# Optimization experiments

Hardware: AMD Instinct MI355X
Metric: run time of the kernel (lower is better)

Reference implementation:

```python
import jax, jax.numpy as jnp
import numpy as np

B, ID, OD = 4096, 2048, 1024


def _conv_softmax(x, w):
    # x: [..., L]; torch Conv1d(1,1,k=3,stride=1,pad=1,bias=False) then softmax(dim=-1)
    L = x.shape[-1]
    xp = jnp.pad(x, [(0, 0)] * (x.ndim - 1) + [(1, 1)])
    y = w[0] * xp[..., 0:L] + w[1] * xp[..., 1:L + 1] + w[2] * xp[..., 2:L + 2]
    return jax.nn.softmax(y, axis=-1)


def _lstm_cell(x, h, c, Wih, Whh, bih, bhh):
    # torch LSTMCell gate order: i, f, g, o
    g = x @ Wih.T + h @ Whh.T + (bih + bhh)
    i, f, gg, o = jnp.split(g, 4, axis=-1)
    c2 = jax.nn.sigmoid(f) * c + jax.nn.sigmoid(i) * jnp.tanh(gg)
    h2 = jax.nn.sigmoid(o) * jnp.tanh(c2)
    return h2, c2


def _lstm_params(key, in_dim, hid):
    k = 1.0 / np.sqrt(hid)
    ks = jax.random.split(key, 4)
    Wih = jax.random.uniform(ks[0], (4 * hid, in_dim), jnp.float32, -k, k)
    Whh = jax.random.uniform(ks[1], (4 * hid, hid), jnp.float32, -k, k)
    bih = jax.random.uniform(ks[2], (4 * hid,), jnp.float32, -k, k)
    bhh = jax.random.uniform(ks[3], (4 * hid,), jnp.float32, -k, k)
    return Wih, Whh, bih, bhh


def setup_inputs() -> dict:
    key = jax.random.key(0)
    ks = jax.random.split(key, 12)
    spec = jax.random.normal(ks[0], (B, ID), jnp.float32)
    Wih1, Whh1, bih1, bhh1 = _lstm_params(ks[1], ID, OD)
    Wih2, Whh2, bih2, bhh2 = _lstm_params(ks[2], ID // 2, OD // 2)
    Wih3, Whh3, bih3, bhh3 = _lstm_params(ks[3], ID // 4, OD // 4)
    Wih4, Whh4, bih4, bhh4 = _lstm_params(ks[4], ID // 8, OD // 8)
    ck = np.sqrt(1.0 / 3.0)  # Conv1d(1,1,3) init bound
    w2_1h = jax.random.uniform(ks[5], (3,), jnp.float32, -ck, ck)
    w2_1c = jax.random.uniform(ks[6], (3,), jnp.float32, -ck, ck)
    w3_2h = jax.random.uniform(ks[7], (3,), jnp.float32, -ck, ck)
    w3_2c = jax.random.uniform(ks[8], (3,), jnp.float32, -ck, ck)
    w4_3h = jax.random.uniform(ks[9], (3,), jnp.float32, -ck, ck)
    w4_3c = jax.random.uniform(ks[10], (3,), jnp.float32, -ck, ck)
    return dict(spec=spec,
                Wih1=Wih1, Whh1=Whh1, bih1=bih1, bhh1=bhh1,
                Wih2=Wih2, Whh2=Whh2, bih2=bih2, bhh2=bhh2,
                Wih3=Wih3, Whh3=Whh3, bih3=bih3, bhh3=bhh3,
                Wih4=Wih4, Whh4=Whh4, bih4=bih4, bhh4=bhh4,
                w2_1h=w2_1h, w2_1c=w2_1c, w3_2h=w3_2h, w3_2c=w3_2c,
                w4_3h=w4_3h, w4_3c=w4_3c)


def reference(spec, Wih1, Whh1, bih1, bhh1, Wih2, Whh2, bih2, bhh2,
              Wih3, Whh3, bih3, bhh3, Wih4, Whh4, bih4, bhh4,
              w2_1h, w2_1c, w3_2h, w3_2c, w4_3h, w4_3c):
    b = spec.shape[0]
    # Level 4: 8 independent steps, fresh zero state each (torch code passes no hidden)
    x4 = spec.reshape(b, 8, ID // 8)
    z4 = jnp.zeros((b, 8, OD // 8), spec.dtype)
    h4, c4 = _lstm_cell(x4, z4, z4, Wih4, Whh4, bih4, bhh4)   # [b,8,OD/8]
    hb4 = _conv_softmax(h4.reshape(b, 4, OD // 4), w4_3h)      # pairs -> [b,4,OD/4]
    cb4 = _conv_softmax(c4.reshape(b, 4, OD // 4), w4_3c)
    # Level 3: 4 independent steps seeded by level-4 blended states
    x3 = spec.reshape(b, 4, ID // 4)
    h3, c3 = _lstm_cell(x3, hb4, cb4, Wih3, Whh3, bih3, bhh3)  # [b,4,OD/4]
    hb3 = _conv_softmax(h3.reshape(b, 2, OD // 2), w3_2h)      # [b,2,OD/2]
    cb3 = _conv_softmax(c3.reshape(b, 2, OD // 2), w3_2c)
    # Level 2: 2 independent steps
    x2 = spec.reshape(b, 2, ID // 2)
    h2, c2 = _lstm_cell(x2, hb3, cb3, Wih2, Whh2, bih2, bhh2)  # [b,2,OD/2]
    hb2 = _conv_softmax(h2.reshape(b, OD), w2_1h)              # [b,OD]
    cb2 = _conv_softmax(c2.reshape(b, OD), w2_1c)
    # Level 1: single full-resolution step; forward returns out1 = h1
    h1, c1 = _lstm_cell(spec, hb2, cb2, Wih1, Whh1, bih1, bhh1)
    return h1
```

## Files before the change

### kernel.cpp

```cpp
#include <hip/hip_runtime.h>


typedef __bf16 bf16x8 __attribute__((ext_vector_type(8)));
typedef float f32x4 __attribute__((ext_vector_type(4)));
typedef unsigned short u16x4 __attribute__((ext_vector_type(4)));
typedef unsigned short u16x8 __attribute__((ext_vector_type(8)));

#define AS1 __attribute__((address_space(1)))
#define AS3 __attribute__((address_space(3)))

__device__ __forceinline__ unsigned short f2bf(float f) {
    union { float f; unsigned int i; } v; v.f = f;
    unsigned int r = v.i + 0x7fffu + ((v.i >> 16) & 1u);
    return (unsigned short)(r >> 16);
}
__device__ __forceinline__ float bf2f(unsigned short u) {
    union { unsigned int i; float f; } v; v.i = ((unsigned int)u) << 16; return v.f;
}
__device__ __forceinline__ float sigm(float x) { return 1.f / (1.f + __expf(-x)); }
__device__ __forceinline__ float tanh_(float x) { float e = __expf(2.f * x); return 1.f - 2.f / (e + 1.f); }

__global__ __launch_bounds__(256) void cvt_spec4(
    const float* __restrict__ spec, unsigned short* __restrict__ sB,
    unsigned short* __restrict__ X, unsigned short* __restrict__ Y,
    unsigned short* __restrict__ Z, long n4)
{
    const long stride = (long)gridDim.x * blockDim.x;
    for (long i = (long)blockIdx.x * blockDim.x + threadIdx.x; i < n4; i += stride) {
        const float4 v = ((const float4*)spec)[i];
        u16x4 o; o.x = f2bf(v.x); o.y = f2bf(v.y); o.z = f2bf(v.z); o.w = f2bf(v.w);
        ((u16x4*)sB)[i] = o;
        const long b = i >> 9;
        const int c4 = (int)(i & 511);
        *(u16x4*)(X + (b * 4 + (c4 >> 7)) * 768  + ((c4 & 127) << 2)) = o;
        *(u16x4*)(Y + (b * 2 + (c4 >> 8)) * 1536 + ((c4 & 255) << 2)) = o;
        *(u16x4*)(Z + b * 3072 + (c4 << 2)) = o;
    }
}

struct PSeg { const float* src; unsigned short* dst; long g0; int H; int kshift; int dstld; int dstcol; };
struct PArgs { PSeg s[7]; long total; };

__global__ __launch_bounds__(256) void cvt_permW_all(PArgs pa)
{
    const long stride = (long)gridDim.x * blockDim.x;
    for (long gi = (long)blockIdx.x * blockDim.x + threadIdx.x; gi < pa.total; gi += stride) {
        int si = 0;
#pragma unroll
        for (int k = 1; k < 7; ++k) si += (gi >= pa.s[k].g0);
        const PSeg sg = pa.s[si];
        const long i = gi - sg.g0;
        const int kq = 1 << sg.kshift;
        const int p = (int)(i >> sg.kshift);
        const int kk = ((int)i & (kq - 1)) << 2;
        const int o = ((p >> 6) << 4) | (p & 15);
        const int q = (p >> 4) & 3;
        const long r = (long)q * sg.H + o;
        const float4 v = *(const float4*)(sg.src + (r << (sg.kshift + 2)) + kk);
        u16x4 wv; wv.x = f2bf(v.x); wv.y = f2bf(v.y); wv.z = f2bf(v.z); wv.w = f2bf(v.w);
        *(u16x4*)(sg.dst + (long)p * sg.dstld + sg.dstcol + kk) = wv;
    }
}

__global__ __launch_bounds__(256) void bias_all(
    const float* __restrict__ bih1, const float* __restrict__ bhh1,
    const float* __restrict__ bih2, const float* __restrict__ bhh2,
    const float* __restrict__ bih3, const float* __restrict__ bhh3,
    const float* __restrict__ bih4, const float* __restrict__ bhh4,
    float* __restrict__ bs1, float* __restrict__ bs2,
    float* __restrict__ bs3, float* __restrict__ bs4)
{
    const int i = blockIdx.x * 256 + threadIdx.x;
    const float *bih, *bhh; float* dst; int H, j;
    if (i < 4096)      { bih = bih1; bhh = bhh1; dst = bs1; H = 1024; j = i; }
    else if (i < 6144) { bih = bih2; bhh = bhh2; dst = bs2; H = 512;  j = i - 4096; }
    else if (i < 7168) { bih = bih3; bhh = bhh3; dst = bs3; H = 256;  j = i - 6144; }
    else               { bih = bih4; bhh = bhh4; dst = bs4; H = 128;  j = i - 7168; }
    const int o = ((j >> 6) << 4) | (j & 15);
    const int q = (j >> 4) & 3;
    dst[j] = bih[q * H + o] + bhh[q * H + o];
}

#define QUAD(AF, S, NS, BF)                                                                 \
    { _Pragma("unroll") for (int mi = 0; mi < 4; ++mi) {                                    \
        _Pragma("unroll") for (int ni = 0; ni < 2; ++ni) {                                  \
            acc[(S)*4+mi][(NS)*2+ni] = __builtin_amdgcn_mfma_f32_16x16x32_bf16(             \
                AF[mi][0], BF[ni][0], acc[(S)*4+mi][(NS)*2+ni], 0, 0, 0);                   \
            acc[(S)*4+mi][(NS)*2+ni] = __builtin_amdgcn_mfma_f32_16x16x32_bf16(             \
                AF[mi][1], BF[ni][1], acc[(S)*4+mi][(NS)*2+ni], 0, 0, 0);                   \
    } } }

#define GLL(gsrc, loff) __builtin_amdgcn_global_load_lds(                                   \
    (const AS1 void*)(gsrc), (AS3 void*)(lds + (loff)), 16, 0, 0)

#define FENCE asm volatile("" ::: "memory")

template<bool HAS_CIN, bool LAST>
__global__ __launch_bounds__(512, 2) void gemm8(
    const unsigned short* __restrict__ A, const unsigned short* __restrict__ W, const int K,
    const float* __restrict__ bsum, const unsigned short* __restrict__ Cin,
    float* __restrict__ HoutF, unsigned short* __restrict__ HoutB,
    unsigned short* __restrict__ CoutB, const int H)
{
    __shared__ __align__(16) char lds[131072];
    const int t = threadIdx.x;
    const int w = t >> 6, l = t & 63;
    const int wr = w >> 2, wc = w & 3;

    const int GX = gridDim.x, GY = gridDim.y;
    const int nwg = GX * GY;
    const int bid = (int)blockIdx.y * GX + (int)blockIdx.x;
    const int swz = (bid & 7) * (nwg >> 3) + (bid >> 3);
    const int m0 = (swz / GY) * 256, n0 = (swz % GY) * 256;

    const int colsw = ((l & 7) ^ (l >> 3)) * 8;
    const size_t k128 = (size_t)128 * K;
    const size_t aoff0 = (size_t)(m0 + w * 16 + (l >> 3)) * K + colsw;
    const size_t aoff1 = aoff0 + (size_t)8 * K;
    const size_t boff0 = (size_t)(n0 + w * 16 + (l >> 3)) * K + colsw;
    const size_t boff1 = boff0 + (size_t)8 * K;
    const int sd0 = w * 2048 + l * 16;
    const int sd1 = sd0 + 1024;

    const int lr128 = (l & 15) * 128;
    const int sw0 = (((l >> 4)    ) ^ (l & 7)) * 16;
    const int sw1 = (((l >> 4) + 4) ^ (l & 7)) * 16;

    f32x4 acc[8][4];
#pragma unroll
    for (int i = 0; i < 8; ++i)
#pragma unroll
        for (int j = 0; j < 4; ++j) acc[i][j] = (f32x4){0.f, 0.f, 0.f, 0.f};

    const int NT = K >> 6;

    GLL(A + aoff0, sd0);                      GLL(A + aoff1, sd1);
    GLL(A + aoff0 + k128, 16384 + sd0);       GLL(A + aoff1 + k128, 16384 + sd1);
    GLL(W + boff0, 32768 + sd0);              GLL(W + boff1, 32768 + sd1);
    GLL(W + boff0 + k128, 49152 + sd0);       GLL(W + boff1 + k128, 49152 + sd1);
    GLL(W + boff0 + 64, 98304 + sd0);         GLL(W + boff1 + 64, 98304 + sd1);
    GLL(W + boff0 + k128 + 64, 114688 + sd0); GLL(W + boff1 + k128 + 64, 114688 + sd1);

    bf16x8 aLo[4][2], aHi[4][2], bF0[2][2], bF1[2][2];

    for (int tt = 0; tt < NT; ++tt) {
        const int q = tt & 1, qn = q ^ 1;
        const int rbA = (q << 16) + (wr << 14) + lr128;
        const int rbB = (q << 16) + 32768 + wc * 8192 + lr128;
        const bool st1 = (tt + 1 < NT), st2 = (tt + 2 < NT);

        if (st1) { asm volatile("s_waitcnt vmcnt(4)" ::: "memory"); }
        else     { asm volatile("s_waitcnt vmcnt(0)" ::: "memory"); }
        __builtin_amdgcn_s_barrier();
        FENCE;

#pragma unroll
        for (int mi = 0; mi < 4; ++mi) {
            aLo[mi][0] = *(const bf16x8*)(lds + rbA + mi * 2048 + sw0);
            aLo[mi][1] = *(const bf16x8*)(lds + rbA + mi * 2048 + sw1);
        }
#pragma unroll
        for (int ni = 0; ni < 2; ++ni) {
            bF0[ni][0] = *(const bf16x8*)(lds + rbB + ni * 2048 + sw0);
            bF0[ni][1] = *(const bf16x8*)(lds + rbB + ni * 2048 + sw1);
            bF1[ni][0] = *(const bf16x8*)(lds + rbB + 4096 + ni * 2048 + sw0);
            bF1[ni][1] = *(const bf16x8*)(lds + rbB + 4096 + ni * 2048 + sw1);
        }
        if (st1) {
            const size_t ko1 = (size_t)(tt + 1) * 64;
            GLL(A + aoff0 + ko1, (qn << 16) + sd0);
            GLL(A + aoff1 + ko1, (qn << 16) + sd1);
            GLL(A + aoff0 + k128 + ko1, (qn << 16) + 16384 + sd0);
            GLL(A + aoff1 + k128 + ko1, (qn << 16) + 16384 + sd1);
        }
#pragma unroll
        for (int mi = 0; mi < 4; ++mi) {
            aHi[mi][0] = *(const bf16x8*)(lds + rbA + 8192 + mi * 2048 + sw0);
            aHi[mi][1] = *(const bf16x8*)(lds + rbA + 8192 + mi * 2048 + sw1);
        }

        __builtin_amdgcn_s_setprio(1);
        QUAD(aLo, 0, 0, bF0);
        QUAD(aLo, 0, 1, bF1);
        __builtin_amdgcn_s_setprio(0);
        __builtin_amdgcn_s_barrier();
        FENCE;

        if (st2) {
            const size_t ko2 = (size_t)(tt + 2) * 64;
            GLL(W + boff0 + ko2, (q << 16) + 32768 + sd0);
            GLL(W + boff1 + ko2, (q << 16) + 32768 + sd1);
            GLL(W + boff0 + k128 + ko2, (q << 16) + 49152 + sd0);
            GLL(W + boff1 + k128 + ko2, (q << 16) + 49152 + sd1);
        }
        __builtin_amdgcn_s_setprio(1);
        QUAD(aHi, 1, 1, bF1);
        QUAD(aHi, 1, 0, bF0);
        __builtin_amdgcn_s_setprio(0);
    }

    const int ocol = (n0 >> 6) * 16 + wc * 16 + (l & 15);
    const int bb = n0 + wc * 64 + (l & 15);
    const float b0 = bsum[bb], b1 = bsum[bb + 16], b2 = bsum[bb + 32], b3 = bsum[bb + 48];
    const int mrow0 = m0 + wr * 128 + (l >> 4) * 4;
#pragma unroll
    for (int mi = 0; mi < 8; ++mi)
#pragma unroll
        for (int j = 0; j < 4; ++j) {
            const size_t m = (size_t)(mrow0 + mi * 16 + j);
            const float gi = acc[mi][0][j] + b0;
            const float gf = acc[mi][1][j] + b1;
            const float gg = acc[mi][2][j] + b2;
            const float go = acc[mi][3][j] + b3;
            float c2 = sigm(gi) * tanh_(gg);
            if (HAS_CIN) c2 += sigm(gf) * bf2f(Cin[m * H + ocol]);
            const float h2 = sigm(go) * tanh_(c2);
            if (LAST) {
                HoutF[m * H + ocol] = h2;
            } else {
                HoutB[m * H + ocol] = f2bf(h2);
                CoutB[m * H + ocol] = f2bf(c2);
            }
        }
}

template<int L>
__global__ __launch_bounds__(256) void conv_dual(
    const unsigned short* __restrict__ Hin, const unsigned short* __restrict__ Cin,
    const float* __restrict__ w3h, const float* __restrict__ w3c,
    unsigned short* __restrict__ Yb, int ldYb, unsigned short* __restrict__ cbuf)
{
    constexpr int R = 2048 / L;
    constexpr int TPR = L / 8;
    __shared__ float xs[R][L + 2];
    __shared__ float red[8];
    const int nb = gridDim.x >> 1;
    const bool isC = (int)blockIdx.x >= nb;
    const int row0 = (isC ? (int)blockIdx.x - nb : (int)blockIdx.x) * R;
    const unsigned short* Xs = isC ? Cin : Hin;
    const float* w3 = isC ? w3c : w3h;
    const int t = threadIdx.x;
    const int r = t / TPR;
    const int c8 = (t % TPR) * 8;
    const float w0 = w3[0], w1 = w3[1], w2 = w3[2];

    const u16x8 v = *(const u16x8*)(Xs + (size_t)(row0 + r) * L + c8);
#pragma unroll
    for (int k = 0; k < 8; ++k) xs[r][c8 + 1 + k] = bf2f(v[k]);
    if (t < R) { xs[t][0] = 0.f; xs[t][L + 1] = 0.f; }
    __syncthreads();

    float y[8];
    float vmax = -3.4e38f;
#pragma unroll
    for (int k = 0; k < 8; ++k) {
        y[k] = w0 * xs[r][c8 + k] + w1 * xs[r][c8 + k + 1] + w2 * xs[r][c8 + k + 2];
        vmax = fmaxf(vmax, y[k]);
    }
#pragma unroll
    for (int off = (TPR >= 64 ? 32 : TPR / 2); off >= 1; off >>= 1)
        vmax = fmaxf(vmax, __shfl_xor(vmax, off));
    if (TPR == 128) {
        if ((t & 63) == 0) red[t >> 6] = vmax;
        __syncthreads();
        vmax = fmaxf(red[2 * r], red[2 * r + 1]);
    }
    float s = 0.f;
#pragma unroll
    for (int k = 0; k < 8; ++k) { y[k] = __expf(y[k] - vmax); s += y[k]; }
#pragma unroll
    for (int off = (TPR >= 64 ? 32 : TPR / 2); off >= 1; off >>= 1)
        s += __shfl_xor(s, off);
    if (TPR == 128) {
        if ((t & 63) == 0) red[4 + (t >> 6)] = s;
        __syncthreads();
        s = red[4 + 2 * r] + red[4 + 2 * r + 1];
    }
    const float inv = 1.f / s;
    u16x8 o;
#pragma unroll
    for (int k = 0; k < 8; ++k) o[k] = f2bf(y[k] * inv);
    if (isC) *(u16x8*)(cbuf + (size_t)(row0 + r) * L + c8) = o;
    else     *(u16x8*)(Yb + (size_t)(row0 + r) * ldYb + c8) = o;
}

extern "C" void kernel_launch(void* const* d_in, const int* in_sizes, int n_in,
                              void* d_out, int out_size, void* d_ws, size_t ws_size,
                              hipStream_t stream)
{
    (void)in_sizes; (void)n_in; (void)out_size; (void)ws_size;
    const float* spec  = (const float*)d_in[0];
    const float* Wih1  = (const float*)d_in[1];
    const float* Whh1  = (const float*)d_in[2];
    const float* bih1  = (const float*)d_in[3];
    const float* bhh1  = (const float*)d_in[4];
    const float* Wih2  = (const float*)d_in[5];
    const float* Whh2  = (const float*)d_in[6];
    const float* bih2  = (const float*)d_in[7];
    const float* bhh2  = (const float*)d_in[8];
    const float* Wih3  = (const float*)d_in[9];
    const float* Whh3  = (const float*)d_in[10];
    const float* bih3  = (const float*)d_in[11];
    const float* bhh3  = (const float*)d_in[12];
    const float* Wih4  = (const float*)d_in[13];
    const float* bih4  = (const float*)d_in[15];
    const float* bhh4  = (const float*)d_in[16];
    const float* w2_1h = (const float*)d_in[17];
    const float* w2_1c = (const float*)d_in[18];
    const float* w3_2h = (const float*)d_in[19];
    const float* w3_2c = (const float*)d_in[20];
    const float* w4_3h = (const float*)d_in[21];
    const float* w4_3c = (const float*)d_in[22];

    char* ws = (char*)d_ws;
    unsigned short* h   = (unsigned short*)(ws + 0);
    unsigned short* c   = (unsigned short*)(ws + (size_t)8388608);
    unsigned short* cb  = (unsigned short*)(ws + (size_t)16777216);
    unsigned short* sB  = (unsigned short*)(ws + (size_t)25165824);
    unsigned short* X   = (unsigned short*)(ws + (size_t)41943040);
    unsigned short* Y   = (unsigned short*)(ws + (size_t)67108864);
    unsigned short* Z   = (unsigned short*)(ws + (size_t)92274688);
    unsigned short* Wc1 = (unsigned short*)(ws + (size_t)117440512);
    unsigned short* Wc2 = (unsigned short*)(ws + (size_t)142606336);
    unsigned short* Wc3 = (unsigned short*)(ws + (size_t)148897792);
    unsigned short* W4  = (unsigned short*)(ws + (size_t)150470656);
    float*          bs1 = (float*)(ws + (size_t)150732800);
    float*          bs2 = bs1 + 4096;
    float*          bs3 = bs2 + 4096;
    float*          bs4 = bs3 + 4096;

    cvt_spec4<<<2048, 256, 0, stream>>>(spec, sB, X, Y, Z, 2097152);
    PArgs pa;
    pa.s[0] = { Wih1, Wc1,       0, 1024, 9, 3072,    0 };
    pa.s[1] = { Whh1, Wc1, 2097152, 1024, 8, 3072, 2048 };
    pa.s[2] = { Wih2, Wc2, 3145728,  512, 8, 1536,    0 };
    pa.s[3] = { Whh2, Wc2, 3670016,  512, 7, 1536, 1024 };
    pa.s[4] = { Wih3, Wc3, 3932160,  256, 7,  768,    0 };
    pa.s[5] = { Whh3, Wc3, 4063232,  256, 6,  768,  512 };
    pa.s[6] = { Wih4, W4,  4128768,  128, 6,  256,    0 };
    pa.total = 4161536;
    cvt_permW_all<<<2048, 256, 0, stream>>>(pa);
    bias_all<<<30, 256, 0, stream>>>(bih1, bhh1, bih2, bhh2, bih3, bhh3, bih4, bhh4,
                                     bs1, bs2, bs3, bs4);

    gemm8<false, false><<<dim3(128, 2), 512, 0, stream>>>(sB, W4, 256, bs4, nullptr,
                                                          nullptr, h, c, 128);
    conv_dual<256><<<4096, 256, 0, stream>>>(h, c, w4_3h, w4_3c, X + 512, 768, cb);

    gemm8<true, false><<<dim3(64, 4), 512, 0, stream>>>(X, Wc3, 768, bs3, cb,
                                                        nullptr, h, c, 256);
    conv_dual<512><<<4096, 256, 0, stream>>>(h, c, w3_2h, w3_2c, Y + 1024, 1536, cb);

    gemm8<true, false><<<dim3(32, 8), 512, 0, stream>>>(Y, Wc2, 1536, bs2, cb,
                                                        nullptr, h, c, 512);
    conv_dual<1024><<<4096, 256, 0, stream>>>(h, c, w2_1h, w2_1c, Z + 2048, 3072, cb);

    gemm8<true, true><<<dim3(16, 16), 512, 0, stream>>>(Z, Wc1, 3072, bs1, cb,
                                                        (float*)d_out, nullptr, nullptr, 1024);
}
```

Baseline: 277.8 us.

## Read GEMM A operand from two sources instead of materialised concatenated buffers

The GEMM now takes two A pointers, spec in bf16 and the blended hidden state, and picks the source per K tile. This removes the X/Y/Z concatenation copies of spec and the strided writes into them. The spec conversion, weight permutation and bias summation are also merged into a single prep kernel, cutting two launches. The trade is extra branching and address arithmetic in the GEMM staging loop.

```diff
diff --git a/kernel.cpp b/kernel.cpp
--- a/kernel.cpp
+++ b/kernel.cpp
@@ -20,74 +20,62 @@
 __device__ __forceinline__ float sigm(float x) { return 1.f / (1.f + __expf(-x)); }
 __device__ __forceinline__ float tanh_(float x) { float e = __expf(2.f * x); return 1.f - 2.f / (e + 1.f); }
 
-__global__ __launch_bounds__(256) void cvt_spec4(
-    const float* __restrict__ spec, unsigned short* __restrict__ sB,
-    unsigned short* __restrict__ X, unsigned short* __restrict__ Y,
-    unsigned short* __restrict__ Z, long n4)
+struct PSeg { const float* src; unsigned short* dst; long g0; int H; int kshift; int dstld; int dstcol; };
+struct PArgs {
+    PSeg s[7];
+    const float* spec; unsigned short* sB;
+    const float *bi1, *bh1, *bi2, *bh2, *bi3, *bh3, *bi4, *bh4;
+    float *bs1, *bs2, *bs3, *bs4;
+};
+
+__global__ __launch_bounds__(256) void prep_all(PArgs pa)
 {
+    const long NS = 2097152;
+    const long NP = 4161536;
+    const long total = NS + NP + 7680;
     const long stride = (long)gridDim.x * blockDim.x;
-    for (long i = (long)blockIdx.x * blockDim.x + threadIdx.x; i < n4; i += stride) {
-        const float4 v = ((const float4*)spec)[i];
-        u16x4 o; o.x = f2bf(v.x); o.y = f2bf(v.y); o.z = f2bf(v.z); o.w = f2bf(v.w);
-        ((u16x4*)sB)[i] = o;
-        const long b = i >> 9;
-        const int c4 = (int)(i & 511);
-        *(u16x4*)(X + (b * 4 + (c4 >> 7)) * 768  + ((c4 & 127) << 2)) = o;
-        *(u16x4*)(Y + (b * 2 + (c4 >> 8)) * 1536 + ((c4 & 255) << 2)) = o;
-        *(u16x4*)(Z + b * 3072 + (c4 << 2)) = o;
-    }
-}
-
-struct PSeg { const float* src; unsigned short* dst; long g0; int H; int kshift; int dstld; int dstcol; };
-struct PArgs { PSeg s[7]; long total; };
-
-__global__ __launch_bounds__(256) void cvt_permW_all(PArgs pa)
-{
-    const long stride = (long)gridDim.x * blockDim.x;
-    for (long gi = (long)blockIdx.x * blockDim.x + threadIdx.x; gi < pa.total; gi += stride) {
-        int si = 0;
-#pragma unroll
-        for (int k = 1; k < 7; ++k) si += (gi >= pa.s[k].g0);
-        const PSeg sg = pa.s[si];
-        const long i = gi - sg.g0;
-        const int kq = 1 << sg.kshift;
-        const int p = (int)(i >> sg.kshift);
-        const int kk = ((int)i & (kq - 1)) << 2;
-        const int o = ((p >> 6) << 4) | (p & 15);
-        const int q = (p >> 4) & 3;
-        const long r = (long)q * sg.H + o;
-        const float4 v = *(const float4*)(sg.src + (r << (sg.kshift + 2)) + kk);
-        u16x4 wv; wv.x = f2bf(v.x); wv.y = f2bf(v.y); wv.z = f2bf(v.z); wv.w = f2bf(v.w);
-        *(u16x4*)(sg.dst + (long)p * sg.dstld + sg.dstcol + kk) = wv;
-    }
-}
-
-__global__ __launch_bounds__(256) void bias_all(
-    const float* __restrict__ bih1, const float* __restrict__ bhh1,
-    const float* __restrict__ bih2, const float* __restrict__ bhh2,
-    const float* __restrict__ bih3, const float* __restrict__ bhh3,
-    const float* __restrict__ bih4, const float* __restrict__ bhh4,
-    float* __restrict__ bs1, float* __restrict__ bs2,
-    float* __restrict__ bs3, float* __restrict__ bs4)
-{
-    const int i = blockIdx.x * 256 + threadIdx.x;
-    const float *bih, *bhh; float* dst; int H, j;
-    if (i < 4096)      { bih = bih1; bhh = bhh1; dst = bs1; H = 1024; j = i; }
-    else if (i < 6144) { bih = bih2; bhh = bhh2; dst = bs2; H = 512;  j = i - 4096; }
-    else if (i < 7168) { bih = bih3; bhh = bhh3; dst = bs3; H = 256;  j = i - 6144; }
-    else               { bih = bih4; bhh = bhh4; dst = bs4; H = 128;  j = i - 7168; }
-    const int o = ((j >> 6) << 4) | (j & 15);
-    const int q = (j >> 4) & 3;
-    dst[j] = bih[q * H + o] + bhh[q * H + o];
-}
-
-#define QUAD(AF, S, NS, BF)                                                                 \
+    for (long gi = (long)blockIdx.x * blockDim.x + threadIdx.x; gi < total; gi += stride) {
+        if (gi < NS) {
+            const float4 v = ((const float4*)pa.spec)[gi];
+            u16x4 o; o.x = f2bf(v.x); o.y = f2bf(v.y); o.z = f2bf(v.z); o.w = f2bf(v.w);
+            ((u16x4*)pa.sB)[gi] = o;
+        } else if (gi < NS + NP) {
+            const long gp = gi - NS;
+            int si = 0;
+#pragma unroll
+            for (int k = 1; k < 7; ++k) si += (gp >= pa.s[k].g0);
+            const PSeg sg = pa.s[si];
+            const long i = gp - sg.g0;
+            const int kq = 1 << sg.kshift;
+            const int p = (int)(i >> sg.kshift);
+            const int kk = ((int)i & (kq - 1)) << 2;
+            const int o = ((p >> 6) << 4) | (p & 15);
+            const int q = (p >> 4) & 3;
+            const long r = (long)q * sg.H + o;
+            const float4 v = *(const float4*)(sg.src + (r << (sg.kshift + 2)) + kk);
+            u16x4 wv; wv.x = f2bf(v.x); wv.y = f2bf(v.y); wv.z = f2bf(v.z); wv.w = f2bf(v.w);
+            *(u16x4*)(sg.dst + (long)p * sg.dstld + sg.dstcol + kk) = wv;
+        } else {
+            const int i = (int)(gi - NS - NP);
+            const float *bih, *bhh; float* dst; int H, j;
+            if (i < 4096)      { bih = pa.bi1; bhh = pa.bh1; dst = pa.bs1; H = 1024; j = i; }
+            else if (i < 6144) { bih = pa.bi2; bhh = pa.bh2; dst = pa.bs2; H = 512;  j = i - 4096; }
+            else if (i < 7168) { bih = pa.bi3; bhh = pa.bh3; dst = pa.bs3; H = 256;  j = i - 6144; }
+            else               { bih = pa.bi4; bhh = pa.bh4; dst = pa.bs4; H = 128;  j = i - 7168; }
+            const int o = ((j >> 6) << 4) | (j & 15);
+            const int q = (j >> 4) & 3;
+            dst[j] = bih[q * H + o] + bhh[q * H + o];
+        }
+    }
+}
+
+#define QUAD(AF, S, NS_, BF)                                                                \
     { _Pragma("unroll") for (int mi = 0; mi < 4; ++mi) {                                    \
         _Pragma("unroll") for (int ni = 0; ni < 2; ++ni) {                                  \
-            acc[(S)*4+mi][(NS)*2+ni] = __builtin_amdgcn_mfma_f32_16x16x32_bf16(             \
-                AF[mi][0], BF[ni][0], acc[(S)*4+mi][(NS)*2+ni], 0, 0, 0);                   \
-            acc[(S)*4+mi][(NS)*2+ni] = __builtin_amdgcn_mfma_f32_16x16x32_bf16(             \
-                AF[mi][1], BF[ni][1], acc[(S)*4+mi][(NS)*2+ni], 0, 0, 0);                   \
+            acc[(S)*4+mi][(NS_)*2+ni] = __builtin_amdgcn_mfma_f32_16x16x32_bf16(            \
+                AF[mi][0], BF[ni][0], acc[(S)*4+mi][(NS_)*2+ni], 0, 0, 0);                  \
+            acc[(S)*4+mi][(NS_)*2+ni] = __builtin_amdgcn_mfma_f32_16x16x32_bf16(            \
+                AF[mi][1], BF[ni][1], acc[(S)*4+mi][(NS_)*2+ni], 0, 0, 0);                  \
     } } }
 
 #define GLL(gsrc, loff) __builtin_amdgcn_global_load_lds(                                   \
@@ -95,9 +83,26 @@
 
 #define FENCE asm volatile("" ::: "memory")
 
+#define STAGE_A(tts, qq)                                                                    \
+    { if ((tts) < nk0) {                                                                    \
+        const size_t ko = (size_t)(tts) * 64;                                               \
+        GLL(A0 + a0off0 + ko, ((qq) << 16) + sd0);                                          \
+        GLL(A0 + a0off1 + ko, ((qq) << 16) + sd1);                                          \
+        GLL(A0 + a0off0 + k128_0 + ko, ((qq) << 16) + 16384 + sd0);                         \
+        GLL(A0 + a0off1 + k128_0 + ko, ((qq) << 16) + 16384 + sd1);                         \
+    } else {                                                                                \
+        const size_t ko = (size_t)((tts) - nk0) * 64;                                       \
+        GLL(A1 + a1off0 + ko, ((qq) << 16) + sd0);                                          \
+        GLL(A1 + a1off1 + ko, ((qq) << 16) + sd1);                                          \
+        GLL(A1 + a1off0 + k128_1 + ko, ((qq) << 16) + 16384 + sd0);                         \
+        GLL(A1 + a1off1 + k128_1 + ko, ((qq) << 16) + 16384 + sd1);                         \
+    } }
+
 template<bool HAS_CIN, bool LAST>
 __global__ __launch_bounds__(512, 2) void gemm8(
-    const unsigned short* __restrict__ A, const unsigned short* __restrict__ W, const int K,
+    const unsigned short* __restrict__ A0, const unsigned short* __restrict__ A1,
+    const int K0, const int K1,
+    const unsigned short* __restrict__ W,
     const float* __restrict__ bsum, const unsigned short* __restrict__ Cin,
     float* __restrict__ HoutF, unsigned short* __restrict__ HoutB,
     unsigned short* __restrict__ CoutB, const int H)
@@ -106,6 +111,8 @@
     const int t = threadIdx.x;
     const int w = t >> 6, l = t & 63;
     const int wr = w >> 2, wc = w & 3;
+    const int K = K0 + K1;
+    const int nk0 = K0 >> 6;
 
     const int GX = gridDim.x, GY = gridDim.y;
     const int nwg = GX * GY;
@@ -114,9 +121,14 @@
     const int m0 = (swz / GY) * 256, n0 = (swz % GY) * 256;
 
     const int colsw = ((l & 7) ^ (l >> 3)) * 8;
+    const int arow = m0 + w * 16 + (l >> 3);
+    const size_t a0off0 = (size_t)arow * K0 + colsw;
+    const size_t a0off1 = a0off0 + (size_t)8 * K0;
+    const size_t a1off0 = (size_t)arow * K1 + colsw;
+    const size_t a1off1 = a1off0 + (size_t)8 * K1;
+    const size_t k128_0 = (size_t)128 * K0;
+    const size_t k128_1 = (size_t)128 * K1;
     const size_t k128 = (size_t)128 * K;
-    const size_t aoff0 = (size_t)(m0 + w * 16 + (l >> 3)) * K + colsw;
-    const size_t aoff1 = aoff0 + (size_t)8 * K;
     const size_t boff0 = (size_t)(n0 + w * 16 + (l >> 3)) * K + colsw;
     const size_t boff1 = boff0 + (size_t)8 * K;
     const int sd0 = w * 2048 + l * 16;
@@ -134,8 +146,7 @@
 
     const int NT = K >> 6;
 
-    GLL(A + aoff0, sd0);                      GLL(A + aoff1, sd1);
-    GLL(A + aoff0 + k128, 16384 + sd0);       GLL(A + aoff1 + k128, 16384 + sd1);
+    STAGE_A(0, 0);
     GLL(W + boff0, 32768 + sd0);              GLL(W + boff1, 32768 + sd1);
     GLL(W + boff0 + k128, 49152 + sd0);       GLL(W + boff1 + k128, 49152 + sd1);
     GLL(W + boff0 + 64, 98304 + sd0);         GLL(W + boff1 + 64, 98304 + sd1);
@@ -166,13 +177,7 @@
             bF1[ni][0] = *(const bf16x8*)(lds + rbB + 4096 + ni * 2048 + sw0);
             bF1[ni][1] = *(const bf16x8*)(lds + rbB + 4096 + ni * 2048 + sw1);
         }
-        if (st1) {
-            const size_t ko1 = (size_t)(tt + 1) * 64;
-            GLL(A + aoff0 + ko1, (qn << 16) + sd0);
-            GLL(A + aoff1 + ko1, (qn << 16) + sd1);
-            GLL(A + aoff0 + k128 + ko1, (qn << 16) + 16384 + sd0);
-            GLL(A + aoff1 + k128 + ko1, (qn << 16) + 16384 + sd1);
-        }
+        if (st1) { STAGE_A(tt + 1, qn); }
 #pragma unroll
         for (int mi = 0; mi < 4; ++mi) {
             aHi[mi][0] = *(const bf16x8*)(lds + rbA + 8192 + mi * 2048 + sw0);
@@ -228,7 +233,7 @@
 __global__ __launch_bounds__(256) void conv_dual(
     const unsigned short* __restrict__ Hin, const unsigned short* __restrict__ Cin,
     const float* __restrict__ w3h, const float* __restrict__ w3c,
-    unsigned short* __restrict__ Yb, int ldYb, unsigned short* __restrict__ cbuf)
+    unsigned short* __restrict__ hbuf, unsigned short* __restrict__ cbuf)
 {
     constexpr int R = 2048 / L;
     constexpr int TPR = L / 8;
@@ -281,7 +286,7 @@
 #pragma unroll
     for (int k = 0; k < 8; ++k) o[k] = f2bf(y[k] * inv);
     if (isC) *(u16x8*)(cbuf + (size_t)(row0 + r) * L + c8) = o;
-    else     *(u16x8*)(Yb + (size_t)(row0 + r) * ldYb + c8) = o;
+    else     *(u16x8*)(hbuf + (size_t)(row0 + r) * L + c8) = o;
 }
 
 extern "C" void kernel_launch(void* const* d_in, const int* in_sizes, int n_in,
@@ -316,20 +321,17 @@
     unsigned short* h   = (unsigned short*)(ws + 0);
     unsigned short* c   = (unsigned short*)(ws + (size_t)8388608);
     unsigned short* cb  = (unsigned short*)(ws + (size_t)16777216);
-    unsigned short* sB  = (unsigned short*)(ws + (size_t)25165824);
-    unsigned short* X   = (unsigned short*)(ws + (size_t)41943040);
-    unsigned short* Y   = (unsigned short*)(ws + (size_t)67108864);
-    unsigned short* Z   = (unsigned short*)(ws + (size_t)92274688);
-    unsigned short* Wc1 = (unsigned short*)(ws + (size_t)117440512);
-    unsigned short* Wc2 = (unsigned short*)(ws + (size_t)142606336);
-    unsigned short* Wc3 = (unsigned short*)(ws + (size_t)148897792);
-    unsigned short* W4  = (unsigned short*)(ws + (size_t)150470656);
-    float*          bs1 = (float*)(ws + (size_t)150732800);
+    unsigned short* hb  = (unsigned short*)(ws + (size_t)25165824);
+    unsigned short* sB  = (unsigned short*)(ws + (size_t)33554432);
+    unsigned short* Wc1 = (unsigned short*)(ws + (size_t)50331648);
+    unsigned short* Wc2 = (unsigned short*)(ws + (size_t)75497472);
+    unsigned short* Wc3 = (unsigned short*)(ws + (size_t)81788928);
+    unsigned short* W4  = (unsigned short*)(ws + (size_t)83361792);
+    float*          bs1 = (float*)(ws + (size_t)83623936);
     float*          bs2 = bs1 + 4096;
     float*          bs3 = bs2 + 4096;
     float*          bs4 = bs3 + 4096;
 
-    cvt_spec4<<<2048, 256, 0, stream>>>(spec, sB, X, Y, Z, 2097152);
     PArgs pa;
     pa.s[0] = { Wih1, Wc1,       0, 1024, 9, 3072,    0 };
     pa.s[1] = { Whh1, Wc1, 2097152, 1024, 8, 3072, 2048 };
@@ -338,23 +340,24 @@
     pa.s[4] = { Wih3, Wc3, 3932160,  256, 7,  768,    0 };
     pa.s[5] = { Whh3, Wc3, 4063232,  256, 6,  768,  512 };
     pa.s[6] = { Wih4, W4,  4128768,  128, 6,  256,    0 };
-    pa.total = 4161536;
-    cvt_permW_all<<<2048, 256, 0, stream>>>(pa);
-    bias_all<<<30, 256, 0, stream>>>(bih1, bhh1, bih2, bhh2, bih3, bhh3, bih4, bhh4,
-                                     bs1, bs2, bs3, bs4);
-
-    gemm8<false, false><<<dim3(128, 2), 512, 0, stream>>>(sB, W4, 256, bs4, nullptr,
-                                                          nullptr, h, c, 128);
-    conv_dual<256><<<4096, 256, 0, stream>>>(h, c, w4_3h, w4_3c, X + 512, 768, cb);
-
-    gemm8<true, false><<<dim3(64, 4), 512, 0, stream>>>(X, Wc3, 768, bs3, cb,
-                                                        nullptr, h, c, 256);
-    conv_dual<512><<<4096, 256, 0, stream>>>(h, c, w3_2h, w3_2c, Y + 1024, 1536, cb);
-
-    gemm8<true, false><<<dim3(32, 8), 512, 0, stream>>>(Y, Wc2, 1536, bs2, cb,
-                                                        nullptr, h, c, 512);
-    conv_dual<1024><<<4096, 256, 0, stream>>>(h, c, w2_1h, w2_1c, Z + 2048, 3072, cb);
-
-    gemm8<true, true><<<dim3(16, 16), 512, 0, stream>>>(Z, Wc1, 3072, bs1, cb,
-                                                        (float*)d_out, nullptr, nullptr, 1024);
-}
+    pa.spec = spec; pa.sB = sB;
+    pa.bi1 = bih1; pa.bh1 = bhh1; pa.bi2 = bih2; pa.bh2 = bhh2;
+    pa.bi3 = bih3; pa.bh3 = bhh3; pa.bi4 = bih4; pa.bh4 = bhh4;
+    pa.bs1 = bs1; pa.bs2 = bs2; pa.bs3 = bs3; pa.bs4 = bs4;
+    prep_all<<<2048, 256, 0, stream>>>(pa);
+
+    gemm8<false, false><<<dim3(128, 2), 512, 0, stream>>>(
+        sB, nullptr, 256, 0, W4, bs4, nullptr, nullptr, h, c, 128);
+    conv_dual<256><<<4096, 256, 0, stream>>>(h, c, w4_3h, w4_3c, hb, cb);
+
+    gemm8<true, false><<<dim3(64, 4), 512, 0, stream>>>(
+        sB, hb, 512, 256, Wc3, bs3, cb, nullptr, h, c, 256);
+    conv_dual<512><<<4096, 256, 0, stream>>>(h, c, w3_2h, w3_2c, hb, cb);
+
+    gemm8<true, false><<<dim3(32, 8), 512, 0, stream>>>(
+        sB, hb, 1024, 512, Wc2, bs2, cb, nullptr, h, c, 512);
+    conv_dual<1024><<<4096, 256, 0, stream>>>(h, c, w2_1h, w2_1c, hb, cb);
+
+    gemm8<true, true><<<dim3(16, 16), 512, 0, stream>>>(
+        sB, hb, 2048, 1024, Wc1, bs1, cb, (float*)d_out, nullptr, nullptr, 1024);
+}
```

New measurement: 271.4 us (median of 3 runs). 2.3% less time.
